# Performance work log

Hardware: AMD Instinct MI355X
Metric: run time of the kernel (lower is better)

The kernel has to match this reference:

```python
import jax, jax.numpy as jnp
import numpy as np

# BHS_GCN: two GCNConv layers (symmetric-normalized gather/scatter-add with
# self-loops, PyG gcn_norm semantics) + dueling value/advantage heads.
# The shared edge list is applied per batch element (vectorized over batch).

N_NODES = 4096
N_HEADS = 3  # len(num_actions)


def gcn_conv(x, src, dst, edge_weight, W, b):
    # x: [B, N, Fin] -> [B, N, Fout]
    n = x.shape[1]
    # degree with self-loop weight 1 (PyG gcn_norm, improved=False)
    deg = jnp.zeros((n,), x.dtype).at[dst].add(edge_weight) + 1.0
    dinv_sqrt = jax.lax.rsqrt(deg)
    norm = edge_weight * dinv_sqrt[src] * dinv_sqrt[dst]  # [E]
    h = x @ W  # [B, N, Fout]
    msg = h[:, src, :] * norm[None, :, None]  # gather + scale
    agg = jnp.zeros_like(h).at[:, dst, :].add(msg)  # scatter-add
    agg = agg + h * (dinv_sqrt * dinv_sqrt)[None, :, None]  # self-loop term 1/deg
    return agg + b


def setup_inputs() -> dict:
    key = jax.random.key(0)
    ks = jax.random.split(key, 16)
    B, N, F, E = 32, N_NODES, 16, 16384
    feat = N * 256
    x = jax.random.normal(ks[0], (B, N, F), dtype=jnp.float32)
    edge_index = jax.random.randint(ks[1], (2, E), 0, N, dtype=jnp.int64)
    edge_weight = jax.random.uniform(ks[2], (E,), dtype=jnp.float32)
    def lin(k, fin, fout):
        return jax.random.normal(k, (fin, fout), dtype=jnp.float32) / np.sqrt(fin)
    return {
        "x": x, "edge_index": edge_index, "edge_weight": edge_weight,
        "W1": lin(ks[3], F, 128), "b1": jnp.zeros((128,), jnp.float32),
        "W2": lin(ks[4], 128, 256), "b2": jnp.zeros((256,), jnp.float32),
        "advW": lin(ks[5], feat, 12), "advb": jnp.zeros((12,), jnp.float32),
        "v1W": lin(ks[6], feat, 64), "v1b": jnp.zeros((64,), jnp.float32),
        "v2W": lin(ks[7], 64, 64), "v2b": jnp.zeros((64,), jnp.float32),
        "v3W": lin(ks[8], 64, 1), "v3b": jnp.zeros((1,), jnp.float32),
    }


def reference(x, edge_index, edge_weight, W1, b1, W2, b2, advW, advb,
              v1W, v1b, v2W, v2b, v3W, v3b):
    src, dst = edge_index[0], edge_index[1]
    h = jax.nn.relu(gcn_conv(x, src, dst, edge_weight, W1, b1))
    h = jax.nn.relu(gcn_conv(h, src, dst, edge_weight, W2, b2))
    B = x.shape[0]
    feat = h.reshape(B, -1)  # [B, N*256]
    adv = jax.nn.relu(feat @ advW + advb).reshape(B, N_HEADS, -1)  # [B, 3, 4]
    val = jax.nn.relu(feat @ v1W + v1b)
    val = jax.nn.relu(val @ v2W + v2b)
    val = val @ v3W + v3b  # [B, 1]
    return val[:, :, None] + adv - adv.mean(-1, keepdims=True)
```

## Files before the change

### kernel.cpp

```cpp
#include <hip/hip_runtime.h>

constexpr int NB = 32;
constexpr int NN = 4096;
constexpr int NE = 16384;
constexpr int NOUT_PAD = 2432;

__device__ __forceinline__ float relu_(float x) { return fmaxf(x, 0.0f); }

__global__ void k_init(float* deg, int* cnt, int* fill) {
  int i = blockIdx.x * 256 + threadIdx.x;
  if (i < NN) { deg[i] = 1.0f; cnt[i] = 0; fill[i] = 0; }
}

__global__ void k_edge1(const int* __restrict__ ei, const float* __restrict__ ew,
                        float* deg, int* cnt) {
  int e = blockIdx.x * 256 + threadIdx.x;
  if (e < NE) {
    int d = ei[NE + e];
    atomicAdd(&deg[d], ew[e]);
    atomicAdd(&cnt[d], 1);
  }
}

__global__ void k_scan(const float* __restrict__ deg, float* __restrict__ dinv,
                       const int* __restrict__ cnt, int* __restrict__ csr_off) {
  __shared__ int sd[1024];
  int t = threadIdx.x;
  int base = t * 4;
  int c0 = cnt[base], c1 = cnt[base+1], c2 = cnt[base+2], c3 = cnt[base+3];
  int s = c0 + c1 + c2 + c3;
  sd[t] = s;
  __syncthreads();
  for (int off = 1; off < 1024; off <<= 1) {
    int v = (t >= off) ? sd[t - off] : 0;
    __syncthreads();
    sd[t] += v;
    __syncthreads();
  }
  int excl = sd[t] - s;
  csr_off[base]     = excl;
  csr_off[base + 1] = excl + c0;
  csr_off[base + 2] = excl + c0 + c1;
  csr_off[base + 3] = excl + c0 + c1 + c2;
  if (t == 1023) csr_off[4096] = sd[1023];
  for (int i = base; i < base + 4; ++i) dinv[i] = rsqrtf(deg[i]);
}

__global__ void k_fill(const int* __restrict__ ei, const float* __restrict__ ew,
                       const float* __restrict__ dinv, const int* __restrict__ csr_off,
                       int* fill, int* __restrict__ csr_src, float* __restrict__ csr_w) {
  int e = blockIdx.x * 256 + threadIdx.x;
  if (e < NE) {
    int s = ei[e], d = ei[NE + e];
    float wn = ew[e] * dinv[s] * dinv[d];
    int p = csr_off[d] + atomicAdd(&fill[d], 1);
    csr_src[p] = s;
    csr_w[p] = wn;
  }
}

__global__ __launch_bounds__(256) void k_agg16(
    const float* __restrict__ x, const float* __restrict__ dinv,
    const int* __restrict__ csr_off, const int* __restrict__ csr_src,
    const float* __restrict__ csr_w, float* __restrict__ g0) {
  int b = blockIdx.y;
  int nn = threadIdx.x >> 4, f = threadIdx.x & 15;
  int n = blockIdx.x * 16 + nn;
  float di = dinv[n];
  size_t base = ((size_t)b * NN + n) * 16;
  float acc = x[base + f] * di * di;
  int e0 = csr_off[n], e1 = csr_off[n + 1];
  for (int e = e0; e < e1; ++e)
    acc = fmaf(csr_w[e], x[((size_t)b * NN + csr_src[e]) * 16 + f], acc);
  g0[base + f] = acc;
}

__global__ __launch_bounds__(256) void k_gemm1(
    const float* __restrict__ g0, const float* __restrict__ W1,
    const float* __restrict__ b1, float* __restrict__ h1) {
  __shared__ float W1s[16 * 128];
  __shared__ float g0s[256];
  int b = blockIdx.y, tile = blockIdx.x, t = threadIdx.x;
  for (int i = t; i < 2048; i += 256) W1s[i] = W1[i];
  g0s[t] = g0[((size_t)b * NN + tile * 16) * 16 + t];
  __syncthreads();
  int k = t & 127, ng = t >> 7;
  float wreg[16];
#pragma unroll
  for (int f = 0; f < 16; ++f) wreg[f] = W1s[f * 128 + k];
  float bias = b1[k];
#pragma unroll
  for (int nn = 0; nn < 8; ++nn) {
    int nl = ng * 8 + nn;
    float acc = bias;
#pragma unroll
    for (int f = 0; f < 16; ++f) acc = fmaf(g0s[nl * 16 + f], wreg[f], acc);
    h1[((size_t)b * NN + tile * 16 + nl) * 128 + k] = relu_(acc);
  }
}

__global__ __launch_bounds__(256) void k_agg128(
    const float* __restrict__ h1, const float* __restrict__ dinv,
    const int* __restrict__ csr_off, const int* __restrict__ csr_src,
    const float* __restrict__ csr_w, float* __restrict__ g1) {
  int b = blockIdx.y;
  int nn = threadIdx.x >> 7, c = threadIdx.x & 127;
  int n = blockIdx.x * 2 + nn;
  float di = dinv[n];
  float acc = h1[((size_t)b * NN + n) * 128 + c] * di * di;
  int e0 = csr_off[n], e1 = csr_off[n + 1];
  for (int e = e0; e < e1; ++e)
    acc = fmaf(csr_w[e], h1[((size_t)b * NN + csr_src[e]) * 128 + c], acc);
  g1[((size_t)b * NN + n) * 128 + c] = acc;
}

__global__ __launch_bounds__(256) void k_gemm2(
    const float* __restrict__ g1, const float* __restrict__ W2,
    const float* __restrict__ b2, float* __restrict__ h2T) {
  __shared__ float g1s[32 * 256];
  int t = threadIdx.x;
  int n0 = blockIdx.x * 2;
  for (int i = t; i < 8192; i += 256) {
    int b = i >> 8, r = i & 255;
    g1s[i] = g1[((size_t)b * NN + n0) * 128 + r];
  }
  __syncthreads();
  int jq = t & 63, bg = t >> 6, b0 = bg * 8;
  const float4* W2v = (const float4*)W2;
  const float2* g1s2 = (const float2*)g1s;
  float4 bv = ((const float4*)b2)[jq];
  for (int nn = 0; nn < 2; ++nn) {
    float acc[8][4];
#pragma unroll
    for (int bb = 0; bb < 8; ++bb) {
      acc[bb][0] = bv.x; acc[bb][1] = bv.y; acc[bb][2] = bv.z; acc[bb][3] = bv.w;
    }
    for (int c = 0; c < 128; c += 2) {
      float4 wA = W2v[c * 64 + jq];
      float4 wB = W2v[(c + 1) * 64 + jq];
#pragma unroll
      for (int bb = 0; bb < 8; ++bb) {
        float2 f2 = g1s2[(b0 + bb) * 128 + nn * 64 + (c >> 1)];
        acc[bb][0] = fmaf(wA.x, f2.x, acc[bb][0]); acc[bb][0] = fmaf(wB.x, f2.y, acc[bb][0]);
        acc[bb][1] = fmaf(wA.y, f2.x, acc[bb][1]); acc[bb][1] = fmaf(wB.y, f2.y, acc[bb][1]);
        acc[bb][2] = fmaf(wA.z, f2.x, acc[bb][2]); acc[bb][2] = fmaf(wB.z, f2.y, acc[bb][2]);
        acc[bb][3] = fmaf(wA.w, f2.x, acc[bb][3]); acc[bb][3] = fmaf(wB.w, f2.y, acc[bb][3]);
      }
    }
#pragma unroll
    for (int jj = 0; jj < 4; ++jj) {
      float4 lo, hi;
      lo.x = relu_(acc[0][jj]); lo.y = relu_(acc[1][jj]); lo.z = relu_(acc[2][jj]); lo.w = relu_(acc[3][jj]);
      hi.x = relu_(acc[4][jj]); hi.y = relu_(acc[5][jj]); hi.z = relu_(acc[6][jj]); hi.w = relu_(acc[7][jj]);
      float* dst0 = h2T + ((size_t)(n0 + nn) * 256 + jq * 4 + jj) * 32 + b0;
      *(float4*)dst0 = lo;
      *(float4*)(dst0 + 4) = hi;
    }
  }
}

__global__ __launch_bounds__(256) void k_head(
    const float* __restrict__ h2T, const float* __restrict__ v1W,
    const float* __restrict__ advW, float* __restrict__ P) {
  __shared__ float s[8192];
  int t = threadIdx.x;
  size_t f0 = (size_t)blockIdx.x * 256;
  const float4* src = (const float4*)(h2T + f0 * 32);
  float4* dst = (float4*)s;
#pragma unroll
  for (int i = 0; i < 8; ++i) dst[t + 256 * i] = src[t + 256 * i];
  __syncthreads();
  int l = t & 63, w = t >> 6;
  bool adv_act = (l < 12);
  float accv[32], acca[32];
#pragma unroll
  for (int i = 0; i < 32; ++i) { accv[i] = 0.0f; acca[i] = 0.0f; }
  const float* v1p  = v1W  + (f0 + (size_t)w * 64) * 64 + l;
  const float* advp = advW + (f0 + (size_t)w * 64) * 12 + l;
#pragma unroll 2
  for (int i = 0; i < 64; ++i) {
    float wv = v1p[i * 64];
    float wa = adv_act ? advp[i * 12] : 0.0f;
    const float4* fr = (const float4*)&s[(w * 64 + i) * 32];
#pragma unroll
    for (int bb = 0; bb < 8; ++bb) {
      float4 h = fr[bb];
      accv[4 * bb + 0] = fmaf(h.x, wv, accv[4 * bb + 0]);
      accv[4 * bb + 1] = fmaf(h.y, wv, accv[4 * bb + 1]);
      accv[4 * bb + 2] = fmaf(h.z, wv, accv[4 * bb + 2]);
      accv[4 * bb + 3] = fmaf(h.w, wv, accv[4 * bb + 3]);
      acca[4 * bb + 0] = fmaf(h.x, wa, acca[4 * bb + 0]);
      acca[4 * bb + 1] = fmaf(h.y, wa, acca[4 * bb + 1]);
      acca[4 * bb + 2] = fmaf(h.z, wa, acca[4 * bb + 2]);
      acca[4 * bb + 3] = fmaf(h.w, wa, acca[4 * bb + 3]);
    }
  }
  float* Pb = P + (size_t)blockIdx.x * NOUT_PAD;
  __syncthreads();
#pragma unroll
  for (int b = 0; b < 32; ++b) s[w * 2048 + b * 64 + l] = accv[b];
  __syncthreads();
  for (int o = t; o < 2048; o += 256)
    Pb[o] = s[o] + s[2048 + o] + s[4096 + o] + s[6144 + o];
  __syncthreads();
  if (adv_act) {
#pragma unroll
    for (int b = 0; b < 32; ++b) s[w * 384 + b * 12 + l] = acca[b];
  }
  __syncthreads();
  for (int o = t; o < 384; o += 256)
    Pb[2048 + o] = s[o] + s[384 + o] + s[768 + o] + s[1152 + o];
}

__global__ __launch_bounds__(256) void k_red1(const float* __restrict__ P,
                                              float* __restrict__ P1) {
  int r = blockIdx.x, t = threadIdx.x;
  const float* p = P + (size_t)r * 64 * NOUT_PAD;
  for (int o = t; o < NOUT_PAD; o += 256) {
    float sum = 0.0f;
    for (int k = 0; k < 64; ++k) sum += p[(size_t)k * NOUT_PAD + o];
    P1[r * NOUT_PAD + o] = sum;
  }
}

__global__ __launch_bounds__(256) void k_red2(const float* __restrict__ P1,
                                              float* __restrict__ S) {
  int o = blockIdx.x * 256 + threadIdx.x;
  if (o >= NOUT_PAD) return;
  float sum = 0.0f;
  for (int r = 0; r < 64; ++r) sum += P1[(size_t)r * NOUT_PAD + o];
  S[o] = sum;
}

__global__ void k_final(const float* __restrict__ S,
                        const float* __restrict__ v1b, const float* __restrict__ v2W,
                        const float* __restrict__ v2b, const float* __restrict__ v3W,
                        const float* __restrict__ v3b, const float* __restrict__ advb,
                        float* __restrict__ out) {
  int b = blockIdx.x, t = threadIdx.x;
  __shared__ float v1s[64], v2s[64], as_[12];
  __shared__ float v3s;
  v1s[t] = relu_(S[b * 64 + t] + v1b[t]);
  if (t < 12) as_[t] = relu_(S[2048 + b * 12 + t] + advb[t]);
  __syncthreads();
  float acc = v2b[t];
  for (int k = 0; k < 64; ++k) acc = fmaf(v1s[k], v2W[k * 64 + t], acc);
  v2s[t] = relu_(acc);
  __syncthreads();
  if (t == 0) {
    float v3 = v3b[0];
    for (int j = 0; j < 64; ++j) v3 = fmaf(v2s[j], v3W[j], v3);
    v3s = v3;
  }
  __syncthreads();
  if (t < 12) {
    int h = t >> 2;
    float m = 0.25f * (as_[h * 4] + as_[h * 4 + 1] + as_[h * 4 + 2] + as_[h * 4 + 3]);
    out[b * 12 + t] = v3s + as_[t] - m;
  }
}

extern "C" void kernel_launch(void* const* d_in, const int* in_sizes, int n_in,
                              void* d_out, int out_size, void* d_ws, size_t ws_size,
                              hipStream_t stream) {
  (void)in_sizes; (void)n_in; (void)out_size; (void)ws_size;
  const float* x    = (const float*)d_in[0];
  const int*   ei   = (const int*)d_in[1];
  const float* ew   = (const float*)d_in[2];
  const float* W1   = (const float*)d_in[3];
  const float* b1   = (const float*)d_in[4];
  const float* W2   = (const float*)d_in[5];
  const float* b2   = (const float*)d_in[6];
  const float* advW = (const float*)d_in[7];
  const float* advb = (const float*)d_in[8];
  const float* v1W  = (const float*)d_in[9];
  const float* v1b  = (const float*)d_in[10];
  const float* v2W  = (const float*)d_in[11];
  const float* v2b  = (const float*)d_in[12];
  const float* v3W  = (const float*)d_in[13];
  const float* v3b  = (const float*)d_in[14];
  float* out = (float*)d_out;

  const size_t MB = 1024 * 1024;
  char* w8 = (char*)d_ws;
  float* deg     = (float*)w8;
  float* dinv    = deg + 4096;
  int*   csr_off = (int*)(dinv + 4096);
  int*   cnt     = csr_off + 4352;
  int*   fill    = cnt + 4096;
  int*   csr_src = fill + 4096;
  float* csr_w   = (float*)(csr_src + NE);
  float* S       = csr_w + NE;
  float* h1  = (float*)(w8 + 4 * MB);
  float* g0  = (float*)(w8 + 68 * MB);
  float* h2T = (float*)(w8 + 4 * MB);
  float* g1  = (float*)(w8 + 132 * MB);
  float* P   = (float*)(w8 + 132 * MB);
  float* P1  = (float*)(w8 + 172 * MB);

  k_init  <<<16, 256, 0, stream>>>(deg, cnt, fill);
  k_edge1 <<<64, 256, 0, stream>>>(ei, ew, deg, cnt);
  k_scan  <<<1, 1024, 0, stream>>>(deg, dinv, cnt, csr_off);
  k_fill  <<<64, 256, 0, stream>>>(ei, ew, dinv, csr_off, fill, csr_src, csr_w);
  k_agg16 <<<dim3(NN / 16, NB), 256, 0, stream>>>(x, dinv, csr_off, csr_src, csr_w, g0);
  k_gemm1 <<<dim3(NN / 16, NB), 256, 0, stream>>>(g0, W1, b1, h1);
  k_agg128<<<dim3(NN / 2, NB), 256, 0, stream>>>(h1, dinv, csr_off, csr_src, csr_w, g1);
  k_gemm2 <<<NN / 2, 256, 0, stream>>>(g1, W2, b2, h2T);
  k_head  <<<NN, 256, 0, stream>>>(h2T, v1W, advW, P);
  k_red1  <<<64, 256, 0, stream>>>(P, P1);
  k_red2  <<<10, 256, 0, stream>>>(P1, S);
  k_final <<<NB, 64, 0, stream>>>(S, v1b, v2W, v2b, v3W, v3b, advb, out);
}
```

Baseline: 801.9 us.

## Run layer-2 GEMM on bf16 MFMA with node-major bf16 aggregation output

Replaces the FP32 FMA layer-2 GEMM with a bf16 MFMA 16x16x32 kernel. The aggregation kernel now writes bf16 output in a node-major layout ([node][batch][channel]) so each block can stream contiguous per-node tiles, and W2 is transposed and cast to bf16 by a new prep kernel each call. The goal is to cut compute time in the GEMM and halve the traffic for the intermediate. In exchange, activations and weights lose precision in bf16, and the h2T stores become scalar strided writes.

```diff
diff --git a/kernel.cpp b/kernel.cpp
--- a/kernel.cpp
+++ b/kernel.cpp
@@ -1,11 +1,19 @@
 #include <hip/hip_runtime.h>
+#include <hip/hip_bf16.h>
 
 constexpr int NB = 32;
 constexpr int NN = 4096;
 constexpr int NE = 16384;
 constexpr int NOUT_PAD = 2432;
 
+typedef __attribute__((ext_vector_type(8))) short short8;
+typedef __attribute__((ext_vector_type(4))) float floatx4;
+
 __device__ __forceinline__ float relu_(float x) { return fmaxf(x, 0.0f); }
+__device__ __forceinline__ unsigned short bf16_(float x) {
+  __hip_bfloat16 h = __float2bfloat16(x);
+  return __builtin_bit_cast(unsigned short, h);
+}
 
 __global__ void k_init(float* deg, int* cnt, int* fill) {
   int i = blockIdx.x * 256 + threadIdx.x;
@@ -57,6 +65,12 @@
     csr_src[p] = s;
     csr_w[p] = wn;
   }
+}
+
+__global__ void k_prep(const float* __restrict__ W2, unsigned short* __restrict__ W2T) {
+  int idx = blockIdx.x * 256 + threadIdx.x;
+  int j = idx >> 7, c = idx & 127;
+  W2T[idx] = bf16_(W2[c * 256 + j]);
 }
 
 __global__ __launch_bounds__(256) void k_agg16(
@@ -102,7 +116,7 @@
 __global__ __launch_bounds__(256) void k_agg128(
     const float* __restrict__ h1, const float* __restrict__ dinv,
     const int* __restrict__ csr_off, const int* __restrict__ csr_src,
-    const float* __restrict__ csr_w, float* __restrict__ g1) {
+    const float* __restrict__ csr_w, unsigned short* __restrict__ g1b) {
   int b = blockIdx.y;
   int nn = threadIdx.x >> 7, c = threadIdx.x & 127;
   int n = blockIdx.x * 2 + nn;
@@ -111,50 +125,73 @@
   int e0 = csr_off[n], e1 = csr_off[n + 1];
   for (int e = e0; e < e1; ++e)
     acc = fmaf(csr_w[e], h1[((size_t)b * NN + csr_src[e]) * 128 + c], acc);
-  g1[((size_t)b * NN + n) * 128 + c] = acc;
-}
-
-__global__ __launch_bounds__(256) void k_gemm2(
-    const float* __restrict__ g1, const float* __restrict__ W2,
+  g1b[((size_t)n * NB + b) * 128 + c] = bf16_(acc);
+}
+
+__global__ __launch_bounds__(256) void k_gemm2b(
+    const unsigned short* __restrict__ g1b, const unsigned short* __restrict__ W2T,
     const float* __restrict__ b2, float* __restrict__ h2T) {
-  __shared__ float g1s[32 * 256];
+  __shared__ unsigned short g1s[32][136];
   int t = threadIdx.x;
-  int n0 = blockIdx.x * 2;
-  for (int i = t; i < 8192; i += 256) {
-    int b = i >> 8, r = i & 255;
-    g1s[i] = g1[((size_t)b * NN + n0) * 128 + r];
-  }
-  __syncthreads();
-  int jq = t & 63, bg = t >> 6, b0 = bg * 8;
-  const float4* W2v = (const float4*)W2;
-  const float2* g1s2 = (const float2*)g1s;
-  float4 bv = ((const float4*)b2)[jq];
-  for (int nn = 0; nn < 2; ++nn) {
-    float acc[8][4];
-#pragma unroll
-    for (int bb = 0; bb < 8; ++bb) {
-      acc[bb][0] = bv.x; acc[bb][1] = bv.y; acc[bb][2] = bv.z; acc[bb][3] = bv.w;
+  int l = t & 63, w = t >> 6;
+  int r = l & 15, ql = l >> 4;
+  int n0 = blockIdx.x * 8;
+  short8 afr[4][4];
+#pragma unroll
+  for (int mt = 0; mt < 4; ++mt)
+#pragma unroll
+    for (int kt = 0; kt < 4; ++kt)
+      afr[mt][kt] = *(const short8*)&W2T[((w * 4 + mt) * 16 + r) * 128 + kt * 32 + ql * 8];
+  float bias[4][4];
+#pragma unroll
+  for (int mt = 0; mt < 4; ++mt)
+#pragma unroll
+    for (int rr = 0; rr < 4; ++rr)
+      bias[mt][rr] = b2[(w * 4 + mt) * 16 + ql * 4 + rr];
+  uint4 pf0, pf1;
+  {
+    const uint4* src = (const uint4*)(g1b + (size_t)n0 * NB * 128);
+    pf0 = src[t]; pf1 = src[t + 256];
+  }
+  for (int i = 0; i < 8; ++i) {
+    __syncthreads();
+    *(uint4*)&g1s[t >> 4][(t & 15) * 8] = pf0;
+    {
+      int i1 = t + 256;
+      *(uint4*)&g1s[i1 >> 4][(i1 & 15) * 8] = pf1;
     }
-    for (int c = 0; c < 128; c += 2) {
-      float4 wA = W2v[c * 64 + jq];
-      float4 wB = W2v[(c + 1) * 64 + jq];
-#pragma unroll
-      for (int bb = 0; bb < 8; ++bb) {
-        float2 f2 = g1s2[(b0 + bb) * 128 + nn * 64 + (c >> 1)];
-        acc[bb][0] = fmaf(wA.x, f2.x, acc[bb][0]); acc[bb][0] = fmaf(wB.x, f2.y, acc[bb][0]);
-        acc[bb][1] = fmaf(wA.y, f2.x, acc[bb][1]); acc[bb][1] = fmaf(wB.y, f2.y, acc[bb][1]);
-        acc[bb][2] = fmaf(wA.z, f2.x, acc[bb][2]); acc[bb][2] = fmaf(wB.z, f2.y, acc[bb][2]);
-        acc[bb][3] = fmaf(wA.w, f2.x, acc[bb][3]); acc[bb][3] = fmaf(wB.w, f2.y, acc[bb][3]);
+    if (i + 1 < 8) {
+      const uint4* src = (const uint4*)(g1b + (size_t)(n0 + i + 1) * NB * 128);
+      pf0 = src[t]; pf1 = src[t + 256];
+    }
+    __syncthreads();
+    short8 bfr[2][4];
+#pragma unroll
+    for (int nt = 0; nt < 2; ++nt)
+#pragma unroll
+      for (int kt = 0; kt < 4; ++kt)
+        bfr[nt][kt] = *(const short8*)&g1s[nt * 16 + r][kt * 32 + ql * 8];
+    floatx4 acc[4][2];
+#pragma unroll
+    for (int mt = 0; mt < 4; ++mt)
+#pragma unroll
+      for (int nt = 0; nt < 2; ++nt) {
+        floatx4 a = {0.0f, 0.0f, 0.0f, 0.0f};
+#pragma unroll
+        for (int kt = 0; kt < 4; ++kt)
+          a = __builtin_amdgcn_mfma_f32_16x16x32_bf16(afr[mt][kt], bfr[nt][kt], a, 0, 0, 0);
+        acc[mt][nt] = a;
       }
-    }
-#pragma unroll
-    for (int jj = 0; jj < 4; ++jj) {
-      float4 lo, hi;
-      lo.x = relu_(acc[0][jj]); lo.y = relu_(acc[1][jj]); lo.z = relu_(acc[2][jj]); lo.w = relu_(acc[3][jj]);
-      hi.x = relu_(acc[4][jj]); hi.y = relu_(acc[5][jj]); hi.z = relu_(acc[6][jj]); hi.w = relu_(acc[7][jj]);
-      float* dst0 = h2T + ((size_t)(n0 + nn) * 256 + jq * 4 + jj) * 32 + b0;
-      *(float4*)dst0 = lo;
-      *(float4*)(dst0 + 4) = hi;
+    size_t nodebase = (size_t)(n0 + i) * 256;
+#pragma unroll
+    for (int mt = 0; mt < 4; ++mt) {
+#pragma unroll
+      for (int rr = 0; rr < 4; ++rr) {
+        int j = (w * 4 + mt) * 16 + ql * 4 + rr;
+        float* dst = h2T + (nodebase + j) * 32 + r;
+        dst[0]  = relu_(acc[mt][0][rr] + bias[mt][rr]);
+        dst[16] = relu_(acc[mt][1][rr] + bias[mt][rr]);
+      }
     }
   }
 }
@@ -291,21 +328,23 @@
   int*   csr_src = fill + 4096;
   float* csr_w   = (float*)(csr_src + NE);
   float* S       = csr_w + NE;
-  float* h1  = (float*)(w8 + 4 * MB);
-  float* g0  = (float*)(w8 + 68 * MB);
-  float* h2T = (float*)(w8 + 4 * MB);
-  float* g1  = (float*)(w8 + 132 * MB);
-  float* P   = (float*)(w8 + 132 * MB);
-  float* P1  = (float*)(w8 + 172 * MB);
+  unsigned short* W2T = (unsigned short*)(S + 2432);
+  float* h1           = (float*)(w8 + 4 * MB);
+  float* g0           = (float*)(w8 + 68 * MB);
+  float* h2T          = (float*)(w8 + 4 * MB);
+  unsigned short* g1b = (unsigned short*)(w8 + 132 * MB);
+  float* P            = (float*)(w8 + 165 * MB);
+  float* P1           = (float*)(w8 + 204 * MB);
 
   k_init  <<<16, 256, 0, stream>>>(deg, cnt, fill);
   k_edge1 <<<64, 256, 0, stream>>>(ei, ew, deg, cnt);
   k_scan  <<<1, 1024, 0, stream>>>(deg, dinv, cnt, csr_off);
   k_fill  <<<64, 256, 0, stream>>>(ei, ew, dinv, csr_off, fill, csr_src, csr_w);
+  k_prep  <<<128, 256, 0, stream>>>(W2, W2T);
   k_agg16 <<<dim3(NN / 16, NB), 256, 0, stream>>>(x, dinv, csr_off, csr_src, csr_w, g0);
   k_gemm1 <<<dim3(NN / 16, NB), 256, 0, stream>>>(g0, W1, b1, h1);
-  k_agg128<<<dim3(NN / 2, NB), 256, 0, stream>>>(h1, dinv, csr_off, csr_src, csr_w, g1);
-  k_gemm2 <<<NN / 2, 256, 0, stream>>>(g1, W2, b2, h2T);
+  k_agg128<<<dim3(NN / 2, NB), 256, 0, stream>>>(h1, dinv, csr_off, csr_src, csr_w, g1b);
+  k_gemm2b<<<NN / 8, 256, 0, stream>>>(g1b, W2T, b2, h2T);
   k_head  <<<NN, 256, 0, stream>>>(h2T, v1W, advW, P);
   k_red1  <<<64, 256, 0, stream>>>(P, P1);
   k_red2  <<<10, 256, 0, stream>>>(P1, S);
```

Measured after the change: 711.7 us. 1.13x faster.
